# Performance work log

Measured on AMD Instinct MI355X. Metric: run time of the kernel, lower is better.

## Reference

```python
import jax, jax.numpy as jnp
import numpy as np

D_MODEL = 40; N_LAYER = 256
D_INNER = 80; D_STATE = 16; D_CONV = 4; DT_RANK = 3  # mamba defaults: expand=2, dt_rank=ceil(40/16)
PE_HID = 48; FF_MULT = 4
B, L, N = 1, 400, 65536


def setup_inputs():
    key = jax.random.key(0)
    ks = jax.random.split(key, 16)
    f32 = jnp.float32
    def rn(k, shape, s=0.02):
        return jax.random.normal(k, shape, f32) * s
    inp = {}
    inp['mash_params'] = jax.random.normal(ks[0], (B, L, D_MODEL), f32)
    inp['qry'] = jax.random.uniform(ks[1], (B, N, 3), f32, -1.0, 1.0)
    # stacked per-layer Mamba params (leading dim = N_LAYER)
    inp['l_norm_w'] = jnp.ones((N_LAYER, D_MODEL), f32)
    inp['l_in_w'] = rn(ks[2], (N_LAYER, 2 * D_INNER, D_MODEL), 0.05)
    inp['l_conv_w'] = rn(ks[3], (N_LAYER, D_INNER, D_CONV), 0.2)
    inp['l_conv_b'] = jnp.zeros((N_LAYER, D_INNER), f32)
    inp['l_xproj_w'] = rn(ks[4], (N_LAYER, DT_RANK + 2 * D_STATE, D_INNER), 0.05)
    inp['l_dt_w'] = rn(ks[5], (N_LAYER, D_INNER, DT_RANK), 0.2)
    inp['l_dt_b'] = rn(ks[6], (N_LAYER, D_INNER), 0.5) - 4.0  # softplus -> small dt
    A = jnp.tile(jnp.arange(1, D_STATE + 1, dtype=f32)[None, None, :], (N_LAYER, D_INNER, 1))
    inp['l_A_log'] = jnp.log(A)
    inp['l_D'] = jnp.ones((N_LAYER, D_INNER), f32)
    inp['l_out_w'] = rn(ks[7], (N_LAYER, D_MODEL, D_INNER), 0.05)
    # PointEmbed MLP (Fourier basis is a fixed buffer, built in forward)
    inp['pe_mlp_w'] = rn(ks[8], (D_MODEL, PE_HID + 3), 0.1)
    inp['pe_mlp_b'] = jnp.zeros((D_MODEL,), f32)
    # PreNorm cross-attention (heads=1, dim_head=d_model)
    inp['ca_lnq_w'] = jnp.ones((D_MODEL,), f32); inp['ca_lnq_b'] = jnp.zeros((D_MODEL,), f32)
    inp['ca_lnc_w'] = jnp.ones((D_MODEL,), f32); inp['ca_lnc_b'] = jnp.zeros((D_MODEL,), f32)
    inp['ca_q_w'] = rn(ks[9], (D_MODEL, D_MODEL), 0.1)
    inp['ca_kv_w'] = rn(ks[10], (2 * D_MODEL, D_MODEL), 0.1)
    inp['ca_out_w'] = rn(ks[11], (D_MODEL, D_MODEL), 0.1)
    inp['ca_out_b'] = jnp.zeros((D_MODEL,), f32)
    # PreNorm GEGLU feed-forward
    inp['ff_ln_w'] = jnp.ones((D_MODEL,), f32); inp['ff_ln_b'] = jnp.zeros((D_MODEL,), f32)
    inp['ff_fc1_w'] = rn(ks[12], (2 * FF_MULT * D_MODEL, D_MODEL), 0.1)
    inp['ff_fc1_b'] = jnp.zeros((2 * FF_MULT * D_MODEL,), f32)
    inp['ff_fc2_w'] = rn(ks[13], (D_MODEL, FF_MULT * D_MODEL), 0.1)
    inp['ff_fc2_b'] = jnp.zeros((D_MODEL,), f32)
    inp['out_w'] = rn(ks[14], (1, D_MODEL), 0.1)
    inp['out_b'] = jnp.zeros((1,), f32)
    return inp


def _rmsnorm(x, w, eps=1e-5):
    return x * jax.lax.rsqrt(jnp.mean(x * x, -1, keepdims=True) + eps) * w


def _layernorm(x, w, b, eps=1e-5):
    m = jnp.mean(x, -1, keepdims=True)
    v = jnp.mean((x - m) ** 2, -1, keepdims=True)
    return (x - m) * jax.lax.rsqrt(v + eps) * w + b


def _mamba(u, p):
    # u: [b, l, d_model]
    xz = jnp.einsum('bld,ed->ble', u, p['in_w'])  # [b,l,2*di]
    x, z = jnp.split(xz, 2, -1)
    # depthwise causal conv1d, kernel D_CONV
    xt = jnp.swapaxes(x, 1, 2)  # [b, di, l]
    xc = jax.lax.conv_general_dilated(xt, p['conv_w'][:, None, :], (1,), [(D_CONV - 1, 0)],
                                      feature_group_count=D_INNER)
    x = jax.nn.silu(jnp.swapaxes(xc + p['conv_b'][None, :, None], 1, 2))  # [b,l,di]
    dbc = jnp.einsum('bld,ed->ble', x, p['xproj_w'])  # [b,l,dt_rank+2*ds]
    dtr = dbc[..., :DT_RANK]
    Bm = dbc[..., DT_RANK:DT_RANK + D_STATE]
    Cm = dbc[..., DT_RANK + D_STATE:]
    dt = jax.nn.softplus(jnp.einsum('blr,dr->bld', dtr, p['dt_w']) + p['dt_b'])  # [b,l,di]
    A = -jnp.exp(p['A_log'])  # [di, ds]
    dA = jnp.exp(dt[..., None] * A)                          # [b,l,di,ds]
    dBx = dt[..., None] * Bm[:, :, None, :] * x[..., None]   # [b,l,di,ds]
    def step(h, io):
        a, bx = io
        h = a * h + bx
        return h, h
    h0 = jnp.zeros((u.shape[0], D_INNER, D_STATE), u.dtype)
    _, hs = jax.lax.scan(step, h0, (jnp.moveaxis(dA, 1, 0), jnp.moveaxis(dBx, 1, 0)))
    hs = jnp.moveaxis(hs, 0, 1)  # [b,l,di,ds]
    y = jnp.einsum('blds,bls->bld', hs, Cm) + x * p['D']
    y = y * jax.nn.silu(z)
    return jnp.einsum('bld,ed->ble', y, p['out_w'])


def _forward(mash_params, qry, l_norm_w, l_in_w, l_conv_w, l_conv_b, l_xproj_w, l_dt_w, l_dt_b,
             l_A_log, l_D, l_out_w, pe_mlp_w, pe_mlp_b, ca_lnq_w, ca_lnq_b, ca_lnc_w, ca_lnc_b,
             ca_q_w, ca_kv_w, ca_out_w, ca_out_b, ff_ln_w, ff_ln_b, ff_fc1_w, ff_fc1_b,
             ff_fc2_w, ff_fc2_b, out_w, out_b):
    layer_params = dict(norm_w=l_norm_w, in_w=l_in_w, conv_w=l_conv_w, conv_b=l_conv_b,
                        xproj_w=l_xproj_w, dt_w=l_dt_w, dt_b=l_dt_b, A_log=l_A_log,
                        D=l_D, out_w=l_out_w)
    # Block: residual = x; h = RMSNorm(x); h = Mamba(h); then caller does x = h + residual
    def layer_fn(x, p):
        return x + _mamba(_rmsnorm(x, p['norm_w']), p), None
    x, _ = jax.lax.scan(layer_fn, mash_params, layer_params)
    # PointEmbed: Fourier features with fixed block-diagonal basis
    e = (2.0 ** jnp.arange(PE_HID // 6, dtype=jnp.float32)) * jnp.pi  # [8]
    z0 = jnp.zeros_like(e)
    basis = jnp.stack([jnp.concatenate([e, z0, z0]),
                       jnp.concatenate([z0, e, z0]),
                       jnp.concatenate([z0, z0, e])])  # [3, 24]
    proj = jnp.einsum('bnd,de->bne', qry, basis)
    pe = jnp.concatenate([jnp.sin(proj), jnp.cos(proj), qry], -1)  # [b,n,51]
    q_emb = jnp.einsum('bnf,df->bnd', pe, pe_mlp_w) + pe_mlp_b
    # PreNorm cross-attention (1 head, dim_head = d_model)
    qn = _layernorm(q_emb, ca_lnq_w, ca_lnq_b)
    cn = _layernorm(x, ca_lnc_w, ca_lnc_b)
    q = jnp.einsum('bnd,ed->bne', qn, ca_q_w)
    kv = jnp.einsum('bld,ed->ble', cn, ca_kv_w)
    k, v = jnp.split(kv, 2, -1)
    scale = D_MODEL ** -0.5
    attn = jax.nn.softmax(jnp.einsum('bnd,bld->bnl', q, k) * scale, axis=-1)  # [b,n,l]
    lat = jnp.einsum('bnl,bld->bnd', attn, v)
    lat = jnp.einsum('bnd,ed->bne', lat, ca_out_w) + ca_out_b
    # PreNorm GEGLU feed-forward with residual
    h = _layernorm(lat, ff_ln_w, ff_ln_b)
    a = jnp.einsum('bnd,ed->bne', h, ff_fc1_w) + ff_fc1_b
    x1, g = jnp.split(a, 2, -1)
    ff = jnp.einsum('bnf,df->bnd', x1 * jax.nn.gelu(g, approximate=False), ff_fc2_w) + ff_fc2_b
    lat = lat + ff
    occ = (jnp.einsum('bnd,od->bno', lat, out_w) + out_b)[..., 0]  # [b, n]
    return occ


def reference(mash_params, qry, l_norm_w, l_in_w, l_conv_w, l_conv_b, l_xproj_w, l_dt_w, l_dt_b,
              l_A_log, l_D, l_out_w, pe_mlp_w, pe_mlp_b, ca_lnq_w, ca_lnq_b, ca_lnc_w, ca_lnc_b,
              ca_q_w, ca_kv_w, ca_out_w, ca_out_b, ff_ln_w, ff_ln_b, ff_fc1_w, ff_fc1_b,
              ff_fc2_w, ff_fc2_b, out_w, out_b):
    return _forward(mash_params, qry, l_norm_w, l_in_w, l_conv_w, l_conv_b, l_xproj_w, l_dt_w,
                    l_dt_b, l_A_log, l_D, l_out_w, pe_mlp_w, pe_mlp_b, ca_lnq_w, ca_lnq_b,
                    ca_lnc_w, ca_lnc_b, ca_q_w, ca_kv_w, ca_out_w, ca_out_b, ff_ln_w, ff_ln_b,
                    ff_fc1_w, ff_fc1_b, ff_fc2_w, ff_fc2_b, out_w, out_b)
```

## Files before the change

kernel.cpp:

```cpp
#include <hip/hip_runtime.h>


#define CH 4
#define NCHUNK 100
#define TPB1 320

typedef unsigned long long u64;

__device__ __forceinline__ u64 pack2(float a, float b) {
  return ((u64)__float_as_uint(b) << 32) | (u64)__float_as_uint(a);
}
__device__ __forceinline__ float unplo(u64 a) {
  return __uint_as_float((unsigned)a);
}
__device__ __forceinline__ float unphi(u64 a) {
  return __uint_as_float((unsigned)(a >> 32));
}

__global__ void init_flags(int* __restrict__ flags) {
  int i = blockIdx.x * 256 + threadIdx.x;
  if (i < 256 * 16) flags[i] = 0;
}

__global__ __launch_bounds__(TPB1) void mamba_pipe(
    const float* __restrict__ mash,
    const float* __restrict__ g_norm_w,
    const float* __restrict__ g_in_w,
    const float* __restrict__ g_conv_w,
    const float* __restrict__ g_conv_b,
    const float* __restrict__ g_xp_w,
    const float* __restrict__ g_dt_w,
    const float* __restrict__ g_dt_b,
    const float* __restrict__ g_alog,
    const float* __restrict__ g_D,
    const float* __restrict__ g_out_w,
    float* __restrict__ xb0,
    float* __restrict__ xb1,
    int* __restrict__ flags)
{
  const int layer = blockIdx.x;
  const int tid = threadIdx.x;

  __shared__ float xin[160];
  __shared__ float xz[640];
  __shared__ float xs[320];
  __shared__ float dbc[144];
  __shared__ float yb[320];
  __shared__ float xhist[240];

  const int e_in = tid % 160;
  const int tA = tid / 160;
  float w_in_r[40];
  {
    const float4* g = (const float4*)(g_in_w + layer * 6400 + e_in * 40);
    const float4* nw = (const float4*)(g_norm_w + layer * 40);
#pragma unroll
    for (int k = 0; k < 10; ++k) {
      float4 v = g[k];
      float4 n = nw[k];
      w_in_r[4 * k] = v.x * n.x; w_in_r[4 * k + 1] = v.y * n.y;
      w_in_r[4 * k + 2] = v.z * n.z; w_in_r[4 * k + 3] = v.w * n.w;
    }
  }
  const int d_c = tid % 80;
  const int t_c = tid / 80;
  float cw[4]; float cb;
  {
    float4 v = *(const float4*)(g_conv_w + layer * 320 + d_c * 4);
    cw[0] = v.x; cw[1] = v.y; cw[2] = v.z; cw[3] = v.w;
    cb = g_conv_b[layer * 80 + d_c];
  }
  const int halfp = tid & 1;
  const int p_x = tid >> 1;
  const int t_x = p_x / 35, e_x = p_x % 35;
  float w_xp_r[40];
  if (p_x < 140) {
    const float4* g = (const float4*)(g_xp_w + layer * 2800 + e_x * 80 + halfp * 40);
#pragma unroll
    for (int k = 0; k < 10; ++k) {
      float4 v = g[k];
      w_xp_r[4 * k] = v.x; w_xp_r[4 * k + 1] = v.y;
      w_xp_r[4 * k + 2] = v.z; w_xp_r[4 * k + 3] = v.w;
    }
  }
  const int d_ch = tid >> 2;
  const int qq = tid & 3;
  float negA[4], hst[4];
  {
    float4 v = *(const float4*)(g_alog + layer * 1280 + tid * 4);
    negA[0] = -__expf(v.x); negA[1] = -__expf(v.y);
    negA[2] = -__expf(v.z); negA[3] = -__expf(v.w);
    hst[0] = hst[1] = hst[2] = hst[3] = 0.f;
  }
  const float dtw0 = g_dt_w[layer * 240 + d_ch * 3 + 0];
  const float dtw1 = g_dt_w[layer * 240 + d_ch * 3 + 1];
  const float dtw2 = g_dt_w[layer * 240 + d_ch * 3 + 2];
  const float dtb = g_dt_b[layer * 80 + d_ch];
  const float wD = g_D[layer * 80 + d_ch];
  const int p_o = tid >> 1;
  const int t_o = p_o / 40, e_o = p_o % 40;
  float w_out_r[40];
  {
    const float4* g = (const float4*)(g_out_w + layer * 3200 + e_o * 80 + halfp * 40);
#pragma unroll
    for (int k = 0; k < 10; ++k) {
      float4 v = g[k];
      w_out_r[4 * k] = v.x; w_out_r[4 * k + 1] = v.y;
      w_out_r[4 * k + 2] = v.z; w_out_r[4 * k + 3] = v.w;
    }
  }

  for (int i = tid; i < 240; i += TPB1) xhist[i] = 0.f;
  __syncthreads();

  const float* src = (layer == 0) ? mash : ((layer & 1) ? xb0 : xb1);
  float* dst = (layer & 1) ? xb1 : xb0;
  int* flag_prev = flags + (layer - 1) * 16;
  int* flag_cur = flags + layer * 16;

  for (int c = 0; c < NCHUNK; ++c) {
    const int t0 = c * CH;

    if (layer == 0) {
#pragma unroll
      for (int tt = 0; tt < 2; ++tt) {
        const int t = tA + 2 * tt;
        const float4* sp = (const float4*)(src + (t0 + t) * 40);
        float ss = 0.f, sd = 0.f;
#pragma unroll
        for (int k = 0; k < 10; ++k) {
          float4 v = sp[k];
          ss += v.x * v.x + v.y * v.y + v.z * v.z + v.w * v.w;
          sd += w_in_r[4 * k] * v.x + w_in_r[4 * k + 1] * v.y
              + w_in_r[4 * k + 2] * v.z + w_in_r[4 * k + 3] * v.w;
        }
        xz[t * 160 + e_in] = sd * rsqrtf(ss * (1.f / 40.f) + 1e-5f);
      }
      if (tid < 160) xin[tid] = src[t0 * 40 + tid];
    } else {
      while (__hip_atomic_load(flag_prev, __ATOMIC_RELAXED,
                               __HIP_MEMORY_SCOPE_AGENT) <= c)
        __builtin_amdgcn_s_sleep(1);
#pragma unroll
      for (int tt = 0; tt < 2; ++tt) {
        const int t = tA + 2 * tt;
        const u64* sp = (const u64*)(src + (t0 + t) * 40);
        float ss = 0.f, sd = 0.f;
#pragma unroll
        for (int k = 0; k < 20; ++k) {
          u64 a = __hip_atomic_load(sp + k, __ATOMIC_RELAXED,
                                    __HIP_MEMORY_SCOPE_AGENT);
          float v0 = unplo(a), v1 = unphi(a);
          ss += v0 * v0 + v1 * v1;
          sd += w_in_r[2 * k] * v0 + w_in_r[2 * k + 1] * v1;
        }
        xz[t * 160 + e_in] = sd * rsqrtf(ss * (1.f / 40.f) + 1e-5f);
      }
      if (tid < 80) {
        u64 a = __hip_atomic_load((const u64*)(src + t0 * 40) + tid,
                                  __ATOMIC_RELAXED, __HIP_MEMORY_SCOPE_AGENT);
        xin[2 * tid] = unplo(a);
        xin[2 * tid + 1] = unphi(a);
      }
    }
    __syncthreads();

    {
      float acc = cb;
#pragma unroll
      for (int j = 0; j < 4; ++j) {
        int lt = t_c - 3 + j;
        float xv = (lt >= 0) ? xz[lt * 160 + d_c] : xhist[(lt + 3) * 80 + d_c];
        acc += cw[j] * xv;
      }
      xs[t_c * 80 + d_c] = acc / (1.f + __expf(-acc));
    }
    __syncthreads();

    if (p_x < 140) {
      const float4* xp = (const float4*)&xs[t_x * 80 + halfp * 40];
      float s = 0.f;
#pragma unroll
      for (int k = 0; k < 10; ++k) {
        float4 v = xp[k];
        s += w_xp_r[4 * k] * v.x + w_xp_r[4 * k + 1] * v.y
           + w_xp_r[4 * k + 2] * v.z + w_xp_r[4 * k + 3] * v.w;
      }
      s += __shfl_xor(s, 1);
      if (halfp == 0) dbc[t_x * 36 + e_x] = s;
    } else {
      for (int k = tid - 280; k < 240; k += 40)
        xhist[k] = xz[(1 + k / 80) * 160 + (k % 80)];
    }
    __syncthreads();

#pragma unroll
    for (int t = 0; t < CH; ++t) {
      const float* db = &dbc[t * 36];
      float sdt = dtb + db[0] * dtw0 + db[1] * dtw1 + db[2] * dtw2;
      float dtval = (sdt > 15.f) ? sdt : __logf(1.f + __expf(sdt));
      float xval = xs[t * 80 + d_ch];
      float part = 0.f;
#pragma unroll
      for (int j = 0; j < 4; ++j) {
        int s_i = qq * 4 + j;
        float Bv = db[3 + s_i];
        float Cv = db[19 + s_i];
        hst[j] = __expf(dtval * negA[j]) * hst[j] + dtval * Bv * xval;
        part += hst[j] * Cv;
      }
      part += __shfl_xor(part, 1);
      part += __shfl_xor(part, 2);
      if (qq == 0) {
        float yv = part + xval * wD;
        float z = xz[t * 160 + 80 + d_ch];
        yb[t * 80 + d_ch] = yv * z / (1.f + __expf(-z));
      }
    }
    __syncthreads();

    {
      const float4* yp = (const float4*)&yb[t_o * 80 + halfp * 40];
      float s = 0.f;
#pragma unroll
      for (int k = 0; k < 10; ++k) {
        float4 v = yp[k];
        s += w_out_r[4 * k] * v.x + w_out_r[4 * k + 1] * v.y
           + w_out_r[4 * k + 2] * v.z + w_out_r[4 * k + 3] * v.w;
      }
      s += __shfl_xor(s, 1);
      float r = xin[p_o] + s;
      float r2 = __shfl_xor(r, 2);
      if ((tid & 3) == 0)
        __hip_atomic_store((u64*)(dst + t0 * 40 + p_o), pack2(r, r2),
                           __ATOMIC_RELAXED, __HIP_MEMORY_SCOPE_AGENT);
    }
    __syncthreads();
    if (tid == 0)
      __hip_atomic_store(flag_cur, c + 1, __ATOMIC_RELAXED,
                         __HIP_MEMORY_SCOPE_AGENT);
  }
}

__global__ __launch_bounds__(64) void kv_kernel(
    const float* __restrict__ xfin,
    const float* __restrict__ lnc_w, const float* __restrict__ lnc_b,
    const float* __restrict__ kv_w,
    float* __restrict__ kbuf, float* __restrict__ vbuf)
{
  int t = blockIdx.x;
  int lane = threadIdx.x;
  float x = (lane < 40) ? xfin[t * 40 + lane] : 0.f;
  float s = x;
#pragma unroll
  for (int o = 32; o >= 1; o >>= 1) s += __shfl_xor(s, o);
  float m = s * (1.f / 40.f);
  float dv = (lane < 40) ? (x - m) : 0.f;
  float v2 = dv * dv;
#pragma unroll
  for (int o = 32; o >= 1; o >>= 1) v2 += __shfl_xor(v2, o);
  float rstd = rsqrtf(v2 * (1.f / 40.f) + 1e-5f);
  __shared__ float cn[40];
  if (lane < 40) cn[lane] = dv * rstd * lnc_w[lane] + lnc_b[lane];
  __syncthreads();
  for (int e = lane; e < 80; e += 64) {
    float acc = 0.f;
#pragma unroll
    for (int d = 0; d < 40; ++d) acc += cn[d] * kv_w[e * 40 + d];
    if (e < 40) kbuf[t * 40 + e] = acc;
    else vbuf[t * 40 + (e - 40)] = acc;
  }
}

__global__ __launch_bounds__(256) void query_kernel(
    const float* __restrict__ qry,
    const float* __restrict__ pe_w, const float* __restrict__ pe_b,
    const float* __restrict__ lnq_w, const float* __restrict__ lnq_b,
    const float* __restrict__ qw,
    const float* __restrict__ ow, const float* __restrict__ ob,
    const float* __restrict__ flw, const float* __restrict__ flb,
    const float* __restrict__ w1, const float* __restrict__ b1,
    const float* __restrict__ w2, const float* __restrict__ b2,
    const float* __restrict__ outw, const float* __restrict__ outb,
    const float* __restrict__ kbuf, const float* __restrict__ vbuf,
    float* __restrict__ out)
{
  const int tid = threadIdx.x;
  const int h = __builtin_amdgcn_readfirstlane((tid >> 6) & 1);
  const int pj = tid >> 7;
  const int lane = tid & 63;
  const int n = blockIdx.x * 128 + pj * 64 + lane;
  const int ptn = tid ^ 64;
  __shared__ float colbuf[40 * 256];
  __shared__ float redm[256], redl[256];

  const float qx = qry[n * 3 + 0], qy = qry[n * 3 + 1], qz = qry[n * 3 + 2];

  float qp[40];
#pragma unroll
  for (int d = 0; d < 40; ++d) qp[d] = 0.f;
#pragma unroll
  for (int jj = 0; jj < 4; ++jj) {
    const int j = h * 4 + jj;
    float f = 3.14159265358979323846f * (float)(1 << j);
    float sx, cx, sy, cy, sz, cz;
    __sincosf(qx * f, &sx, &cx);
    __sincosf(qy * f, &sy, &cy);
    __sincosf(qz * f, &sz, &cz);
#pragma unroll
    for (int d = 0; d < 40; ++d) {
      const float* r = pe_w + d * 51;
      qp[d] += sx * r[j] + sy * r[j + 8] + sz * r[j + 16]
             + cx * r[j + 24] + cy * r[j + 32] + cz * r[j + 40];
    }
  }
#pragma unroll
  for (int d = 0; d < 40; ++d) colbuf[d * 256 + tid] = qp[d];
  __syncthreads();
  float qe[40];
#pragma unroll
  for (int d = 0; d < 40; ++d) {
    const float* r = pe_w + d * 51;
    qe[d] = pe_b[d] + qp[d] + colbuf[d * 256 + ptn]
          + qx * r[48] + qy * r[49] + qz * r[50];
  }
  __syncthreads();

  float qn[40];
  {
    float m = 0.f;
#pragma unroll
    for (int d = 0; d < 40; ++d) m += qe[d];
    m *= (1.f / 40.f);
    float var = 0.f;
#pragma unroll
    for (int d = 0; d < 40; ++d) { float dv = qe[d] - m; var += dv * dv; }
    float rstd = rsqrtf(var * (1.f / 40.f) + 1e-5f);
#pragma unroll
    for (int d = 0; d < 40; ++d) qn[d] = (qe[d] - m) * rstd * lnq_w[d] + lnq_b[d];
  }
  float qnh[20];
#pragma unroll
  for (int dd = 0; dd < 20; ++dd) qnh[dd] = h ? qn[dd + 20] : qn[dd];
  float q[40];
#pragma unroll
  for (int e = 0; e < 40; ++e) q[e] = 0.f;
#pragma unroll 1
  for (int dd = 0; dd < 20; ++dd) {
    const float qv = qnh[dd];
    const int d = h * 20 + dd;
#pragma unroll
    for (int e = 0; e < 40; ++e) q[e] += qv * qw[e * 40 + d];
  }
#pragma unroll
  for (int e = 0; e < 40; ++e) colbuf[e * 256 + tid] = q[e];
  __syncthreads();
#pragma unroll
  for (int e = 0; e < 40; ++e) q[e] += colbuf[e * 256 + ptn];
  __syncthreads();

  float acc[40];
#pragma unroll
  for (int d = 0; d < 40; ++d) acc[d] = 0.f;
  float mx = -1e30f, l = 0.f;
  const float scale = 0.15811388300841897f;
  const int tbeg = h * 200, tend = tbeg + 200;
#pragma unroll 1
  for (int t = tbeg; t < tend; ++t) {
    const float4* kr = (const float4*)(kbuf + t * 40);
    float s0 = 0.f, s1 = 0.f, s2 = 0.f, s3 = 0.f;
#pragma unroll
    for (int k = 0; k < 10; ++k) {
      float4 k4 = kr[k];
      s0 += q[4 * k] * k4.x; s1 += q[4 * k + 1] * k4.y;
      s2 += q[4 * k + 2] * k4.z; s3 += q[4 * k + 3] * k4.w;
    }
    float s = ((s0 + s1) + (s2 + s3)) * scale;
    if (s > mx) {
      float corr = __expf(mx - s);
      l *= corr;
#pragma unroll
      for (int d = 0; d < 40; ++d) acc[d] *= corr;
      mx = s;
    }
    float p = __expf(s - mx);
    l += p;
    const float4* vr = (const float4*)(vbuf + t * 40);
#pragma unroll
    for (int k = 0; k < 10; ++k) {
      float4 v4 = vr[k];
      acc[4 * k] += p * v4.x; acc[4 * k + 1] += p * v4.y;
      acc[4 * k + 2] += p * v4.z; acc[4 * k + 3] += p * v4.w;
    }
  }
#pragma unroll
  for (int d = 0; d < 40; ++d) colbuf[d * 256 + tid] = acc[d];
  redm[tid] = mx; redl[tid] = l;
  __syncthreads();
  float lat[40];
  {
    float m2 = redm[ptn];
    float l2 = redl[ptn];
    float nm = fmaxf(mx, m2);
    float a = __expf(mx - nm), b = __expf(m2 - nm);
    float lm = l * a + l2 * b;
    float linv = 1.f / lm;
#pragma unroll
    for (int d = 0; d < 40; ++d)
      lat[d] = (acc[d] * a + colbuf[d * 256 + ptn] * b) * linv;
  }
  __syncthreads();

  float lath[20];
#pragma unroll
  for (int dd = 0; dd < 20; ++dd) lath[dd] = h ? lat[dd + 20] : lat[dd];
  float lp[40];
#pragma unroll
  for (int e = 0; e < 40; ++e) lp[e] = 0.f;
#pragma unroll 1
  for (int dd = 0; dd < 20; ++dd) {
    const float lv = lath[dd];
    const int d = h * 20 + dd;
#pragma unroll
    for (int e = 0; e < 40; ++e) lp[e] += lv * ow[e * 40 + d];
  }
#pragma unroll
  for (int e = 0; e < 40; ++e) colbuf[e * 256 + tid] = lp[e];
  __syncthreads();
  float lat2[40];
#pragma unroll
  for (int e = 0; e < 40; ++e) lat2[e] = ob[e] + lp[e] + colbuf[e * 256 + ptn];
  __syncthreads();

  float hh[40];
  {
    float m = 0.f;
#pragma unroll
    for (int d = 0; d < 40; ++d) m += lat2[d];
    m *= (1.f / 40.f);
    float var = 0.f;
#pragma unroll
    for (int d = 0; d < 40; ++d) { float dv = lat2[d] - m; var += dv * dv; }
    float rstd = rsqrtf(var * (1.f / 40.f) + 1e-5f);
#pragma unroll
    for (int d = 0; d < 40; ++d) hh[d] = (lat2[d] - m) * rstd * flw[d] + flb[d];
  }
  float ff[40];
#pragma unroll
  for (int d = 0; d < 40; ++d) ff[d] = 0.f;
#pragma unroll 1
  for (int ee = 0; ee < 80; ++ee) {
    const int e = h * 80 + ee;
    const float* r1 = w1 + e * 40;
    const float* r2 = w1 + (160 + e) * 40;
    float a0 = 0.f, a1 = 0.f;
#pragma unroll
    for (int d = 0; d < 40; ++d) { a0 += hh[d] * r1[d]; a1 += hh[d] * r2[d]; }
    float x1 = a0 + b1[e];
    float g = a1 + b1[160 + e];
    float tv = x1 * (0.5f * g * (1.f + erff(g * 0.70710678118654752f)));
#pragma unroll
    for (int d = 0; d < 40; ++d) ff[d] += tv * w2[d * 160 + e];
  }
#pragma unroll
  for (int d = 0; d < 40; ++d) colbuf[d * 256 + tid] = ff[d];
  __syncthreads();
  float r = outb[0];
#pragma unroll
  for (int d = 0; d < 40; ++d) {
    float f = ff[d] + colbuf[d * 256 + ptn] + b2[d];
    r += (lat2[d] + f) * outw[d];
  }
  if (h == 0) out[n] = r;
}

extern "C" void kernel_launch(void* const* d_in, const int* in_sizes, int n_in,
                              void* d_out, int out_size, void* d_ws, size_t ws_size,
                              hipStream_t stream) {
  const float* mash   = (const float*)d_in[0];
  const float* qry    = (const float*)d_in[1];
  const float* lnw    = (const float*)d_in[2];
  const float* linw   = (const float*)d_in[3];
  const float* lconvw = (const float*)d_in[4];
  const float* lconvb = (const float*)d_in[5];
  const float* lxpw   = (const float*)d_in[6];
  const float* ldtw   = (const float*)d_in[7];
  const float* ldtb   = (const float*)d_in[8];
  const float* lAlog  = (const float*)d_in[9];
  const float* lD     = (const float*)d_in[10];
  const float* loutw  = (const float*)d_in[11];
  const float* pew    = (const float*)d_in[12];
  const float* peb    = (const float*)d_in[13];
  const float* lnqw   = (const float*)d_in[14];
  const float* lnqb   = (const float*)d_in[15];
  const float* lncw   = (const float*)d_in[16];
  const float* lncb   = (const float*)d_in[17];
  const float* qw     = (const float*)d_in[18];
  const float* kvw    = (const float*)d_in[19];
  const float* oww    = (const float*)d_in[20];
  const float* owb    = (const float*)d_in[21];
  const float* flnw   = (const float*)d_in[22];
  const float* flnb   = (const float*)d_in[23];
  const float* w1     = (const float*)d_in[24];
  const float* b1     = (const float*)d_in[25];
  const float* w2     = (const float*)d_in[26];
  const float* b2     = (const float*)d_in[27];
  const float* outw   = (const float*)d_in[28];
  const float* outb   = (const float*)d_in[29];

  float* wsf = (float*)d_ws;
  float* xb0 = wsf;
  float* xb1 = wsf + 16000;
  float* kbuf = wsf + 32000;
  float* vbuf = wsf + 48000;
  int* flags = (int*)(wsf + 64000);

  hipLaunchKernelGGL(init_flags, dim3(16), dim3(256), 0, stream, flags);
  hipLaunchKernelGGL(mamba_pipe, dim3(256), dim3(TPB1), 0, stream,
                     mash, lnw, linw, lconvw, lconvb, lxpw, ldtw, ldtb, lAlog,
                     lD, loutw, xb0, xb1, flags);
  hipLaunchKernelGGL(kv_kernel, dim3(400), dim3(64), 0, stream,
                     xb1, lncw, lncb, kvw, kbuf, vbuf);
  hipLaunchKernelGGL(query_kernel, dim3(512), dim3(256), 0, stream,
                     qry, pew, peb, lnqw, lnqb, qw, oww, owb, flnw, flnb,
                     w1, b1, w2, b2, outw, outb, kbuf, vbuf, (float*)d_out);
}
```

Measured before the change: 2.168 ms.

## Precompute query projections in spare blocks of the Mamba pipeline kernel

```diff
diff --git a/kernel.cpp b/kernel.cpp
--- a/kernel.cpp
+++ b/kernel.cpp
@@ -36,10 +36,71 @@
     const float* __restrict__ g_out_w,
     float* __restrict__ xb0,
     float* __restrict__ xb1,
-    int* __restrict__ flags)
+    int* __restrict__ flags,
+    const float* __restrict__ qry,
+    const float* __restrict__ pe_w, const float* __restrict__ pe_b,
+    const float* __restrict__ lnq_w, const float* __restrict__ lnq_b,
+    const float* __restrict__ qw,
+    float* __restrict__ qstore)
 {
+  const int tid = threadIdx.x;
+
+  if (blockIdx.x >= 256) {
+    const int n = (blockIdx.x - 256) * TPB1 + tid;
+    if (n < 65536) {
+      const float qx = qry[n * 3 + 0], qy = qry[n * 3 + 1], qz = qry[n * 3 + 2];
+      float qe[40];
+#pragma unroll
+      for (int d = 0; d < 40; ++d) qe[d] = pe_b[d];
+#pragma unroll 1
+      for (int j = 0; j < 8; ++j) {
+        float f = 3.14159265358979323846f * (float)(1 << j);
+        float sx, cx, sy, cy, sz, cz;
+        __sincosf(qx * f, &sx, &cx);
+        __sincosf(qy * f, &sy, &cy);
+        __sincosf(qz * f, &sz, &cz);
+#pragma unroll
+        for (int d = 0; d < 40; ++d) {
+          const float* r = pe_w + d * 51;
+          qe[d] += sx * r[j] + sy * r[j + 8] + sz * r[j + 16]
+                 + cx * r[j + 24] + cy * r[j + 32] + cz * r[j + 40];
+        }
+      }
+#pragma unroll
+      for (int d = 0; d < 40; ++d) {
+        const float* r = pe_w + d * 51;
+        qe[d] += qx * r[48] + qy * r[49] + qz * r[50];
+      }
+      float qn[40];
+      {
+        float m = 0.f;
+#pragma unroll
+        for (int d = 0; d < 40; ++d) m += qe[d];
+        m *= (1.f / 40.f);
+        float var = 0.f;
+#pragma unroll
+        for (int d = 0; d < 40; ++d) { float dv = qe[d] - m; var += dv * dv; }
+        float rstd = rsqrtf(var * (1.f / 40.f) + 1e-5f);
+#pragma unroll
+        for (int d = 0; d < 40; ++d)
+          qn[d] = (qe[d] - m) * rstd * lnq_w[d] + lnq_b[d];
+      }
+      float q[40];
+#pragma unroll
+      for (int e = 0; e < 40; ++e) {
+        const float* r = qw + e * 40;
+        float s = 0.f;
+#pragma unroll
+        for (int d = 0; d < 40; ++d) s += qn[d] * r[d];
+        q[e] = s;
+      }
+#pragma unroll
+      for (int e = 0; e < 40; ++e) qstore[e * 65536 + n] = q[e];
+    }
+    return;
+  }
+
   const int layer = blockIdx.x;
-  const int tid = threadIdx.x;
 
   __shared__ float xin[160];
   __shared__ float xz[640];
@@ -272,7 +333,187 @@
   }
 }
 
-__global__ __launch_bounds__(256) void query_kernel(
+__global__ __launch_bounds__(256) void query_fast(
+    const float* __restrict__ qstore,
+    const float* __restrict__ ow, const float* __restrict__ ob,
+    const float* __restrict__ flw, const float* __restrict__ flb,
+    const float* __restrict__ w1, const float* __restrict__ b1,
+    const float* __restrict__ w2, const float* __restrict__ b2,
+    const float* __restrict__ outw, const float* __restrict__ outb,
+    const float* __restrict__ kbuf, const float* __restrict__ vbuf,
+    float* __restrict__ out)
+{
+  const int tid = threadIdx.x;
+  const int h = __builtin_amdgcn_readfirstlane((tid >> 6) & 3);
+  const int lane = tid & 63;
+  const int n = blockIdx.x * 64 + lane;
+  const int p1 = tid ^ 64, p2 = tid ^ 128, p3 = tid ^ 192;
+  __shared__ float colbuf[40 * 256];
+
+  float q[40];
+#pragma unroll
+  for (int e = 0; e < 40; ++e) q[e] = qstore[e * 65536 + n];
+
+  float acc[40];
+#pragma unroll
+  for (int d = 0; d < 40; ++d) acc[d] = 0.f;
+  float mx = -1e30f, l = 0.f;
+  const float scale = 0.15811388300841897f;
+  const int tbeg = h * 100;
+#pragma unroll 1
+  for (int t = tbeg; t < tbeg + 100; t += 2) {
+    const float4* ka = (const float4*)(kbuf + t * 40);
+    const float4* kb = (const float4*)(kbuf + t * 40 + 40);
+    float a0 = 0.f, a1 = 0.f, b0 = 0.f, b1s = 0.f;
+#pragma unroll
+    for (int k = 0; k < 10; ++k) {
+      float4 k4 = ka[k];
+      float4 j4 = kb[k];
+      a0 += q[4 * k] * k4.x + q[4 * k + 1] * k4.y;
+      a1 += q[4 * k + 2] * k4.z + q[4 * k + 3] * k4.w;
+      b0 += q[4 * k] * j4.x + q[4 * k + 1] * j4.y;
+      b1s += q[4 * k + 2] * j4.z + q[4 * k + 3] * j4.w;
+    }
+    float sa = (a0 + a1) * scale;
+    float sb = (b0 + b1s) * scale;
+    {
+      if (sa > mx) {
+        float corr = __expf(mx - sa);
+        l *= corr;
+#pragma unroll
+        for (int d = 0; d < 40; ++d) acc[d] *= corr;
+        mx = sa;
+      }
+      float p = __expf(sa - mx);
+      l += p;
+      const float4* vr = (const float4*)(vbuf + t * 40);
+#pragma unroll
+      for (int k = 0; k < 10; ++k) {
+        float4 v4 = vr[k];
+        acc[4 * k] += p * v4.x; acc[4 * k + 1] += p * v4.y;
+        acc[4 * k + 2] += p * v4.z; acc[4 * k + 3] += p * v4.w;
+      }
+    }
+    {
+      if (sb > mx) {
+        float corr = __expf(mx - sb);
+        l *= corr;
+#pragma unroll
+        for (int d = 0; d < 40; ++d) acc[d] *= corr;
+        mx = sb;
+      }
+      float p = __expf(sb - mx);
+      l += p;
+      const float4* vr = (const float4*)(vbuf + (t + 1) * 40);
+#pragma unroll
+      for (int k = 0; k < 10; ++k) {
+        float4 v4 = vr[k];
+        acc[4 * k] += p * v4.x; acc[4 * k + 1] += p * v4.y;
+        acc[4 * k + 2] += p * v4.z; acc[4 * k + 3] += p * v4.w;
+      }
+    }
+  }
+
+  {
+    float* redm = colbuf;
+    float* redl = colbuf + 256;
+    redm[tid] = mx; redl[tid] = l;
+  }
+  __syncthreads();
+  float a0c, a1c, a2c, a3c, linv;
+  {
+    float m1 = colbuf[p1], m2 = colbuf[p2], m3 = colbuf[p3];
+    float l1 = colbuf[256 + p1], l2 = colbuf[256 + p2], l3 = colbuf[256 + p3];
+    float nm = fmaxf(fmaxf(mx, m1), fmaxf(m2, m3));
+    a0c = __expf(mx - nm); a1c = __expf(m1 - nm);
+    a2c = __expf(m2 - nm); a3c = __expf(m3 - nm);
+    float L = l * a0c + l1 * a1c + l2 * a2c + l3 * a3c;
+    linv = 1.f / L;
+  }
+  __syncthreads();
+#pragma unroll
+  for (int d = 0; d < 40; ++d) colbuf[d * 256 + tid] = acc[d];
+  __syncthreads();
+  float lat[40];
+#pragma unroll
+  for (int d = 0; d < 40; ++d)
+    lat[d] = (acc[d] * a0c + colbuf[d * 256 + p1] * a1c
+            + colbuf[d * 256 + p2] * a2c + colbuf[d * 256 + p3] * a3c) * linv;
+  __syncthreads();
+
+  float lath[10];
+#pragma unroll
+  for (int dd = 0; dd < 10; ++dd) {
+    float v = lat[dd];
+    v = (h == 1) ? lat[dd + 10] : v;
+    v = (h == 2) ? lat[dd + 20] : v;
+    v = (h == 3) ? lat[dd + 30] : v;
+    lath[dd] = v;
+  }
+  float lp[40];
+#pragma unroll
+  for (int e = 0; e < 40; ++e) lp[e] = 0.f;
+#pragma unroll 1
+  for (int dd = 0; dd < 10; ++dd) {
+    const float lv = lath[dd];
+    const int d = h * 10 + dd;
+#pragma unroll
+    for (int e = 0; e < 40; ++e) lp[e] += lv * ow[e * 40 + d];
+  }
+#pragma unroll
+  for (int e = 0; e < 40; ++e) colbuf[e * 256 + tid] = lp[e];
+  __syncthreads();
+  float lat2[40];
+#pragma unroll
+  for (int e = 0; e < 40; ++e)
+    lat2[e] = ob[e] + lp[e] + colbuf[e * 256 + p1]
+            + colbuf[e * 256 + p2] + colbuf[e * 256 + p3];
+  __syncthreads();
+
+  float hh[40];
+  {
+    float m = 0.f;
+#pragma unroll
+    for (int d = 0; d < 40; ++d) m += lat2[d];
+    m *= (1.f / 40.f);
+    float var = 0.f;
+#pragma unroll
+    for (int d = 0; d < 40; ++d) { float dv = lat2[d] - m; var += dv * dv; }
+    float rstd = rsqrtf(var * (1.f / 40.f) + 1e-5f);
+#pragma unroll
+    for (int d = 0; d < 40; ++d) hh[d] = (lat2[d] - m) * rstd * flw[d] + flb[d];
+  }
+  float ff[40];
+#pragma unroll
+  for (int d = 0; d < 40; ++d) ff[d] = 0.f;
+#pragma unroll 1
+  for (int ee = 0; ee < 40; ++ee) {
+    const int e = h * 40 + ee;
+    const float* r1 = w1 + e * 40;
+    const float* r2 = w1 + (160 + e) * 40;
+    float s0 = 0.f, s1 = 0.f;
+#pragma unroll
+    for (int d = 0; d < 40; ++d) { s0 += hh[d] * r1[d]; s1 += hh[d] * r2[d]; }
+    float x1 = s0 + b1[e];
+    float g = s1 + b1[160 + e];
+    float tv = x1 * (0.5f * g * (1.f + erff(g * 0.70710678118654752f)));
+#pragma unroll
+    for (int d = 0; d < 40; ++d) ff[d] += tv * w2[d * 160 + e];
+  }
+#pragma unroll
+  for (int d = 0; d < 40; ++d) colbuf[d * 256 + tid] = ff[d];
+  __syncthreads();
+  float r = outb[0];
+#pragma unroll
+  for (int d = 0; d < 40; ++d) {
+    float f = ff[d] + colbuf[d * 256 + p1] + colbuf[d * 256 + p2]
+            + colbuf[d * 256 + p3] + b2[d];
+    r += (lat2[d] + f) * outw[d];
+  }
+  if (h == 0) out[n] = r;
+}
+
+__global__ __launch_bounds__(256) void query_kernel_fb(
     const float* __restrict__ qry,
     const float* __restrict__ pe_w, const float* __restrict__ pe_b,
     const float* __restrict__ lnq_w, const float* __restrict__ lnq_b,
@@ -295,7 +536,6 @@
   __shared__ float redm[256], redl[256];
 
   const float qx = qry[n * 3 + 0], qy = qry[n * 3 + 1], qz = qry[n * 3 + 2];
-
   float qp[40];
 #pragma unroll
   for (int d = 0; d < 40; ++d) qp[d] = 0.f;
@@ -325,7 +565,6 @@
           + qx * r[48] + qy * r[49] + qz * r[50];
   }
   __syncthreads();
-
   float qn[40];
   {
     float m = 0.f;
@@ -410,7 +649,6 @@
       lat[d] = (acc[d] * a + colbuf[d * 256 + ptn] * b) * linv;
   }
   __syncthreads();
-
   float lath[20];
 #pragma unroll
   for (int dd = 0; dd < 20; ++dd) lath[dd] = h ? lat[dd + 20] : lat[dd];
@@ -431,7 +669,6 @@
 #pragma unroll
   for (int e = 0; e < 40; ++e) lat2[e] = ob[e] + lp[e] + colbuf[e * 256 + ptn];
   __syncthreads();
-
   float hh[40];
   {
     float m = 0.f;
@@ -453,11 +690,11 @@
     const int e = h * 80 + ee;
     const float* r1 = w1 + e * 40;
     const float* r2 = w1 + (160 + e) * 40;
-    float a0 = 0.f, a1 = 0.f;
-#pragma unroll
-    for (int d = 0; d < 40; ++d) { a0 += hh[d] * r1[d]; a1 += hh[d] * r2[d]; }
-    float x1 = a0 + b1[e];
-    float g = a1 + b1[160 + e];
+    float s0 = 0.f, s1 = 0.f;
+#pragma unroll
+    for (int d = 0; d < 40; ++d) { s0 += hh[d] * r1[d]; s1 += hh[d] * r2[d]; }
+    float x1 = s0 + b1[e];
+    float g = s1 + b1[160 + e];
     float tv = x1 * (0.5f * g * (1.f + erff(g * 0.70710678118654752f)));
 #pragma unroll
     for (int d = 0; d < 40; ++d) ff[d] += tv * w2[d * 160 + e];
@@ -514,14 +751,24 @@
   float* kbuf = wsf + 32000;
   float* vbuf = wsf + 48000;
   int* flags = (int*)(wsf + 64000);
+  float* qstore = wsf + 68096;
+  const size_t needed = (size_t)68096 * 4 + (size_t)40 * 65536 * 4;
+  const bool pre = ws_size >= needed;
 
   hipLaunchKernelGGL(init_flags, dim3(16), dim3(256), 0, stream, flags);
-  hipLaunchKernelGGL(mamba_pipe, dim3(256), dim3(TPB1), 0, stream,
+  hipLaunchKernelGGL(mamba_pipe, dim3(pre ? 461 : 256), dim3(TPB1), 0, stream,
                      mash, lnw, linw, lconvw, lconvb, lxpw, ldtw, ldtb, lAlog,
-                     lD, loutw, xb0, xb1, flags);
+                     lD, loutw, xb0, xb1, flags,
+                     qry, pew, peb, lnqw, lnqb, qw, qstore);
   hipLaunchKernelGGL(kv_kernel, dim3(400), dim3(64), 0, stream,
                      xb1, lncw, lncb, kvw, kbuf, vbuf);
-  hipLaunchKernelGGL(query_kernel, dim3(512), dim3(256), 0, stream,
-                     qry, pew, peb, lnqw, lnqb, qw, oww, owb, flnw, flnb,
-                     w1, b1, w2, b2, outw, outb, kbuf, vbuf, (float*)d_out);
-}
+  if (pre) {
+    hipLaunchKernelGGL(query_fast, dim3(1024), dim3(256), 0, stream,
+                       qstore, oww, owb, flnw, flnb,
+                       w1, b1, w2, b2, outw, outb, kbuf, vbuf, (float*)d_out);
+  } else {
+    hipLaunchKernelGGL(query_kernel_fb, dim3(512), dim3(256), 0, stream,
+                       qry, pew, peb, lnqw, lnqb, qw, oww, owb, flnw, flnb,
+                       w1, b1, w2, b2, outw, outb, kbuf, vbuf, (float*)d_out);
+  }
+}
```

Result: faster. 2.115 ms (-2.4%).

## Fuse KV projection and query attention into the persistent mamba pipeline kernel

Applied to the files above, without the earlier changes.

```diff
diff --git a/kernel.cpp b/kernel.cpp
--- a/kernel.cpp
+++ b/kernel.cpp
@@ -19,10 +19,10 @@
 
 __global__ void init_flags(int* __restrict__ flags) {
   int i = blockIdx.x * 256 + threadIdx.x;
-  if (i < 256 * 16) flags[i] = 0;
+  if (i < 257 * 16) flags[i] = 0;
 }
 
-__global__ __launch_bounds__(TPB1) void mamba_pipe(
+__global__ __launch_bounds__(TPB1, 3) void mamba_pipe(
     const float* __restrict__ mash,
     const float* __restrict__ g_norm_w,
     const float* __restrict__ g_in_w,
@@ -36,9 +36,21 @@
     const float* __restrict__ g_out_w,
     float* __restrict__ xb0,
     float* __restrict__ xb1,
-    int* __restrict__ flags)
+    int* __restrict__ flags,
+    const float* __restrict__ lnc_w, const float* __restrict__ lnc_b,
+    const float* __restrict__ kv_w,
+    float* __restrict__ kbuf, float* __restrict__ vbuf,
+    const float* __restrict__ qry,
+    const float* __restrict__ pe_w, const float* __restrict__ pe_b,
+    const float* __restrict__ lnq_w, const float* __restrict__ lnq_b,
+    const float* __restrict__ qw,
+    const float* __restrict__ ow, const float* __restrict__ ob,
+    const float* __restrict__ flw, const float* __restrict__ flb,
+    const float* __restrict__ w1, const float* __restrict__ b1,
+    const float* __restrict__ w2, const float* __restrict__ b2,
+    const float* __restrict__ outw, const float* __restrict__ outb,
+    float* __restrict__ out)
 {
-  const int layer = blockIdx.x;
   const int tid = threadIdx.x;
 
   __shared__ float xin[160];
@@ -47,6 +59,233 @@
   __shared__ float dbc[144];
   __shared__ float yb[320];
   __shared__ float xhist[240];
+
+  if (blockIdx.x >= 257) {
+    const int waveid = tid >> 6;
+    const int lane = tid & 63;
+    const int wq = (blockIdx.x - 257) * 5 + waveid;
+    if (wq >= 1024) return;
+    const int n = wq * 64 + lane;
+
+    const float qx = qry[n * 3 + 0], qy = qry[n * 3 + 1], qz = qry[n * 3 + 2];
+    float q[40];
+    {
+      float qe[40];
+#pragma unroll
+      for (int d = 0; d < 40; ++d) qe[d] = pe_b[d];
+#pragma unroll 1
+      for (int j = 0; j < 8; ++j) {
+        float f = 3.14159265358979323846f * (float)(1 << j);
+        float sx, cx, sy, cy, sz, cz;
+        __sincosf(qx * f, &sx, &cx);
+        __sincosf(qy * f, &sy, &cy);
+        __sincosf(qz * f, &sz, &cz);
+#pragma unroll
+        for (int d = 0; d < 40; ++d) {
+          const float* r = pe_w + d * 51;
+          qe[d] += sx * r[j] + sy * r[j + 8] + sz * r[j + 16]
+                 + cx * r[j + 24] + cy * r[j + 32] + cz * r[j + 40];
+        }
+      }
+#pragma unroll
+      for (int d = 0; d < 40; ++d) {
+        const float* r = pe_w + d * 51;
+        qe[d] += qx * r[48] + qy * r[49] + qz * r[50];
+      }
+      float m = 0.f;
+#pragma unroll
+      for (int d = 0; d < 40; ++d) m += qe[d];
+      m *= (1.f / 40.f);
+      float var = 0.f;
+#pragma unroll
+      for (int d = 0; d < 40; ++d) { float dv = qe[d] - m; var += dv * dv; }
+      float rstd = rsqrtf(var * (1.f / 40.f) + 1e-5f);
+      float qn[40];
+#pragma unroll
+      for (int d = 0; d < 40; ++d)
+        qn[d] = (qe[d] - m) * rstd * lnq_w[d] + lnq_b[d];
+#pragma unroll
+      for (int e = 0; e < 40; ++e) {
+        const float* r = qw + e * 40;
+        float s = 0.f;
+#pragma unroll
+        for (int d = 0; d < 40; ++d) s += qn[d] * r[d];
+        q[e] = s;
+      }
+    }
+
+    int* kv_flag = flags + 256 * 16;
+    float acc[40];
+#pragma unroll
+    for (int d = 0; d < 40; ++d) acc[d] = 0.f;
+    float mx = -1e30f, l = 0.f;
+    const float scale = 0.15811388300841897f;
+#pragma unroll 1
+    for (int c = 0; c < NCHUNK; ++c) {
+      if (c == 0) {
+        while (__hip_atomic_load(kv_flag, __ATOMIC_RELAXED,
+                                 __HIP_MEMORY_SCOPE_AGENT) <= 0)
+          __builtin_amdgcn_s_sleep(32);
+      } else {
+        while (__hip_atomic_load(kv_flag, __ATOMIC_RELAXED,
+                                 __HIP_MEMORY_SCOPE_AGENT) <= c)
+          __builtin_amdgcn_s_sleep(8);
+      }
+#pragma unroll 1
+      for (int tt = 0; tt < CH; ++tt) {
+        const int t = c * CH + tt;
+        const u64* kp = (const u64*)(kbuf + t * 40);
+        float kvv[40];
+#pragma unroll
+        for (int k = 0; k < 20; ++k) {
+          u64 a = __hip_atomic_load(kp + k, __ATOMIC_RELAXED,
+                                    __HIP_MEMORY_SCOPE_AGENT);
+          kvv[2 * k] = unplo(a); kvv[2 * k + 1] = unphi(a);
+        }
+        float s0 = 0.f, s1 = 0.f, s2 = 0.f, s3 = 0.f;
+#pragma unroll
+        for (int d = 0; d < 40; d += 4) {
+          s0 += q[d] * kvv[d]; s1 += q[d + 1] * kvv[d + 1];
+          s2 += q[d + 2] * kvv[d + 2]; s3 += q[d + 3] * kvv[d + 3];
+        }
+        float s = ((s0 + s1) + (s2 + s3)) * scale;
+        if (s > mx) {
+          float corr = __expf(mx - s);
+          l *= corr;
+#pragma unroll
+          for (int d = 0; d < 40; ++d) acc[d] *= corr;
+          mx = s;
+        }
+        float p = __expf(s - mx);
+        l += p;
+        const u64* vp = (const u64*)(vbuf + t * 40);
+#pragma unroll
+        for (int k = 0; k < 20; ++k) {
+          u64 a = __hip_atomic_load(vp + k, __ATOMIC_RELAXED,
+                                    __HIP_MEMORY_SCOPE_AGENT);
+          acc[2 * k] += p * unplo(a);
+          acc[2 * k + 1] += p * unphi(a);
+        }
+      }
+    }
+
+    float linv = 1.f / l;
+    float lat[40];
+#pragma unroll
+    for (int d = 0; d < 40; ++d) lat[d] = acc[d] * linv;
+    float lat2[40];
+#pragma unroll 1
+    for (int e = 0; e < 40; ++e) {
+      const float* r = ow + e * 40;
+      float s = 0.f;
+#pragma unroll
+      for (int d = 0; d < 40; ++d) s += lat[d] * r[d];
+      lat2[e] = ob[e] + s;
+    }
+    float hh[40];
+    {
+      float m = 0.f;
+#pragma unroll
+      for (int d = 0; d < 40; ++d) m += lat2[d];
+      m *= (1.f / 40.f);
+      float var = 0.f;
+#pragma unroll
+      for (int d = 0; d < 40; ++d) { float dv = lat2[d] - m; var += dv * dv; }
+      float rstd = rsqrtf(var * (1.f / 40.f) + 1e-5f);
+#pragma unroll
+      for (int d = 0; d < 40; ++d)
+        hh[d] = (lat2[d] - m) * rstd * flw[d] + flb[d];
+    }
+    float ff[40];
+#pragma unroll
+    for (int d = 0; d < 40; ++d) ff[d] = b2[d];
+#pragma unroll 1
+    for (int e = 0; e < 160; ++e) {
+      const float* r1 = w1 + e * 40;
+      const float* r2 = w1 + (160 + e) * 40;
+      float a0 = 0.f, a1 = 0.f;
+#pragma unroll
+      for (int d = 0; d < 40; ++d) { a0 += hh[d] * r1[d]; a1 += hh[d] * r2[d]; }
+      float x1 = a0 + b1[e];
+      float g = a1 + b1[160 + e];
+      float tv = x1 * (0.5f * g * (1.f + erff(g * 0.70710678118654752f)));
+#pragma unroll
+      for (int d = 0; d < 40; ++d) ff[d] += tv * w2[d * 160 + e];
+    }
+    float r = outb[0];
+#pragma unroll
+    for (int d = 0; d < 40; ++d) r += (lat2[d] + ff[d]) * outw[d];
+    out[n] = r;
+    return;
+  }
+
+  if (blockIdx.x == 256) {
+    const int t_k = tid / 80;
+    const int e_k = tid % 80;
+    float wkv[40];
+    {
+      const float4* g = (const float4*)(kv_w + e_k * 40);
+#pragma unroll
+      for (int k = 0; k < 10; ++k) {
+        float4 v = g[k];
+        wkv[4 * k] = v.x; wkv[4 * k + 1] = v.y;
+        wkv[4 * k + 2] = v.z; wkv[4 * k + 3] = v.w;
+      }
+    }
+    float lw = 0.f, lb = 0.f;
+    if (tid < 160) { lw = lnc_w[tid % 40]; lb = lnc_b[tid % 40]; }
+    const u64* srcT = (const u64*)xb1;
+    int* flag_src = flags + 255 * 16;
+    int* kv_flag = flags + 256 * 16;
+
+    for (int c = 0; c < NCHUNK; ++c) {
+      while (__hip_atomic_load(flag_src, __ATOMIC_RELAXED,
+                               __HIP_MEMORY_SCOPE_AGENT) <= c)
+        __builtin_amdgcn_s_sleep(1);
+      if (tid < 80) {
+        u64 a = __hip_atomic_load(srcT + c * 80 + tid, __ATOMIC_RELAXED,
+                                  __HIP_MEMORY_SCOPE_AGENT);
+        xz[2 * tid] = unplo(a);
+        xz[2 * tid + 1] = unphi(a);
+      }
+      __syncthreads();
+      if (tid < 160) {
+        const int t = tid / 40;
+        float m = 0.f;
+#pragma unroll
+        for (int k = 0; k < 40; ++k) m += xz[t * 40 + k];
+        m *= (1.f / 40.f);
+        float var = 0.f;
+#pragma unroll
+        for (int k = 0; k < 40; ++k) {
+          float dv = xz[t * 40 + k] - m; var += dv * dv;
+        }
+        float rstd = rsqrtf(var * (1.f / 40.f) + 1e-5f);
+        yb[tid] = (xz[tid] - m) * rstd * lw + lb;
+      }
+      __syncthreads();
+      {
+        const float* cn = &yb[t_k * 40];
+        float s = 0.f;
+#pragma unroll
+        for (int d = 0; d < 40; ++d) s += wkv[d] * cn[d];
+        const int trow = c * CH + t_k;
+        if (e_k < 40)
+          __hip_atomic_store(&kbuf[trow * 40 + e_k], s, __ATOMIC_RELAXED,
+                             __HIP_MEMORY_SCOPE_AGENT);
+        else
+          __hip_atomic_store(&vbuf[trow * 40 + (e_k - 40)], s,
+                             __ATOMIC_RELAXED, __HIP_MEMORY_SCOPE_AGENT);
+      }
+      __syncthreads();
+      if (tid == 0)
+        __hip_atomic_store(kv_flag, c + 1, __ATOMIC_RELAXED,
+                           __HIP_MEMORY_SCOPE_AGENT);
+    }
+    return;
+  }
+
+  const int layer = blockIdx.x;
 
   const int e_in = tid % 160;
   const int tA = tid / 160;
@@ -240,238 +479,6 @@
       __hip_atomic_store(flag_cur, c + 1, __ATOMIC_RELAXED,
                          __HIP_MEMORY_SCOPE_AGENT);
   }
-}
-
-__global__ __launch_bounds__(64) void kv_kernel(
-    const float* __restrict__ xfin,
-    const float* __restrict__ lnc_w, const float* __restrict__ lnc_b,
-    const float* __restrict__ kv_w,
-    float* __restrict__ kbuf, float* __restrict__ vbuf)
-{
-  int t = blockIdx.x;
-  int lane = threadIdx.x;
-  float x = (lane < 40) ? xfin[t * 40 + lane] : 0.f;
-  float s = x;
-#pragma unroll
-  for (int o = 32; o >= 1; o >>= 1) s += __shfl_xor(s, o);
-  float m = s * (1.f / 40.f);
-  float dv = (lane < 40) ? (x - m) : 0.f;
-  float v2 = dv * dv;
-#pragma unroll
-  for (int o = 32; o >= 1; o >>= 1) v2 += __shfl_xor(v2, o);
-  float rstd = rsqrtf(v2 * (1.f / 40.f) + 1e-5f);
-  __shared__ float cn[40];
-  if (lane < 40) cn[lane] = dv * rstd * lnc_w[lane] + lnc_b[lane];
-  __syncthreads();
-  for (int e = lane; e < 80; e += 64) {
-    float acc = 0.f;
-#pragma unroll
-    for (int d = 0; d < 40; ++d) acc += cn[d] * kv_w[e * 40 + d];
-    if (e < 40) kbuf[t * 40 + e] = acc;
-    else vbuf[t * 40 + (e - 40)] = acc;
-  }
-}
-
-__global__ __launch_bounds__(256) void query_kernel(
-    const float* __restrict__ qry,
-    const float* __restrict__ pe_w, const float* __restrict__ pe_b,
-    const float* __restrict__ lnq_w, const float* __restrict__ lnq_b,
-    const float* __restrict__ qw,
-    const float* __restrict__ ow, const float* __restrict__ ob,
-    const float* __restrict__ flw, const float* __restrict__ flb,
-    const float* __restrict__ w1, const float* __restrict__ b1,
-    const float* __restrict__ w2, const float* __restrict__ b2,
-    const float* __restrict__ outw, const float* __restrict__ outb,
-    const float* __restrict__ kbuf, const float* __restrict__ vbuf,
-    float* __restrict__ out)
-{
-  const int tid = threadIdx.x;
-  const int h = __builtin_amdgcn_readfirstlane((tid >> 6) & 1);
-  const int pj = tid >> 7;
-  const int lane = tid & 63;
-  const int n = blockIdx.x * 128 + pj * 64 + lane;
-  const int ptn = tid ^ 64;
-  __shared__ float colbuf[40 * 256];
-  __shared__ float redm[256], redl[256];
-
-  const float qx = qry[n * 3 + 0], qy = qry[n * 3 + 1], qz = qry[n * 3 + 2];
-
-  float qp[40];
-#pragma unroll
-  for (int d = 0; d < 40; ++d) qp[d] = 0.f;
-#pragma unroll
-  for (int jj = 0; jj < 4; ++jj) {
-    const int j = h * 4 + jj;
-    float f = 3.14159265358979323846f * (float)(1 << j);
-    float sx, cx, sy, cy, sz, cz;
-    __sincosf(qx * f, &sx, &cx);
-    __sincosf(qy * f, &sy, &cy);
-    __sincosf(qz * f, &sz, &cz);
-#pragma unroll
-    for (int d = 0; d < 40; ++d) {
-      const float* r = pe_w + d * 51;
-      qp[d] += sx * r[j] + sy * r[j + 8] + sz * r[j + 16]
-             + cx * r[j + 24] + cy * r[j + 32] + cz * r[j + 40];
-    }
-  }
-#pragma unroll
-  for (int d = 0; d < 40; ++d) colbuf[d * 256 + tid] = qp[d];
-  __syncthreads();
-  float qe[40];
-#pragma unroll
-  for (int d = 0; d < 40; ++d) {
-    const float* r = pe_w + d * 51;
-    qe[d] = pe_b[d] + qp[d] + colbuf[d * 256 + ptn]
-          + qx * r[48] + qy * r[49] + qz * r[50];
-  }
-  __syncthreads();
-
-  float qn[40];
-  {
-    float m = 0.f;
-#pragma unroll
-    for (int d = 0; d < 40; ++d) m += qe[d];
-    m *= (1.f / 40.f);
-    float var = 0.f;
-#pragma unroll
-    for (int d = 0; d < 40; ++d) { float dv = qe[d] - m; var += dv * dv; }
-    float rstd = rsqrtf(var * (1.f / 40.f) + 1e-5f);
-#pragma unroll
-    for (int d = 0; d < 40; ++d) qn[d] = (qe[d] - m) * rstd * lnq_w[d] + lnq_b[d];
-  }
-  float qnh[20];
-#pragma unroll
-  for (int dd = 0; dd < 20; ++dd) qnh[dd] = h ? qn[dd + 20] : qn[dd];
-  float q[40];
-#pragma unroll
-  for (int e = 0; e < 40; ++e) q[e] = 0.f;
-#pragma unroll 1
-  for (int dd = 0; dd < 20; ++dd) {
-    const float qv = qnh[dd];
-    const int d = h * 20 + dd;
-#pragma unroll
-    for (int e = 0; e < 40; ++e) q[e] += qv * qw[e * 40 + d];
-  }
-#pragma unroll
-  for (int e = 0; e < 40; ++e) colbuf[e * 256 + tid] = q[e];
-  __syncthreads();
-#pragma unroll
-  for (int e = 0; e < 40; ++e) q[e] += colbuf[e * 256 + ptn];
-  __syncthreads();
-
-  float acc[40];
-#pragma unroll
-  for (int d = 0; d < 40; ++d) acc[d] = 0.f;
-  float mx = -1e30f, l = 0.f;
-  const float scale = 0.15811388300841897f;
-  const int tbeg = h * 200, tend = tbeg + 200;
-#pragma unroll 1
-  for (int t = tbeg; t < tend; ++t) {
-    const float4* kr = (const float4*)(kbuf + t * 40);
-    float s0 = 0.f, s1 = 0.f, s2 = 0.f, s3 = 0.f;
-#pragma unroll
-    for (int k = 0; k < 10; ++k) {
-      float4 k4 = kr[k];
-      s0 += q[4 * k] * k4.x; s1 += q[4 * k + 1] * k4.y;
-      s2 += q[4 * k + 2] * k4.z; s3 += q[4 * k + 3] * k4.w;
-    }
-    float s = ((s0 + s1) + (s2 + s3)) * scale;
-    if (s > mx) {
-      float corr = __expf(mx - s);
-      l *= corr;
-#pragma unroll
-      for (int d = 0; d < 40; ++d) acc[d] *= corr;
-      mx = s;
-    }
-    float p = __expf(s - mx);
-    l += p;
-    const float4* vr = (const float4*)(vbuf + t * 40);
-#pragma unroll
-    for (int k = 0; k < 10; ++k) {
-      float4 v4 = vr[k];
-      acc[4 * k] += p * v4.x; acc[4 * k + 1] += p * v4.y;
-      acc[4 * k + 2] += p * v4.z; acc[4 * k + 3] += p * v4.w;
-    }
-  }
-#pragma unroll
-  for (int d = 0; d < 40; ++d) colbuf[d * 256 + tid] = acc[d];
-  redm[tid] = mx; redl[tid] = l;
-  __syncthreads();
-  float lat[40];
-  {
-    float m2 = redm[ptn];
-    float l2 = redl[ptn];
-    float nm = fmaxf(mx, m2);
-    float a = __expf(mx - nm), b = __expf(m2 - nm);
-    float lm = l * a + l2 * b;
-    float linv = 1.f / lm;
-#pragma unroll
-    for (int d = 0; d < 40; ++d)
-      lat[d] = (acc[d] * a + colbuf[d * 256 + ptn] * b) * linv;
-  }
-  __syncthreads();
-
-  float lath[20];
-#pragma unroll
-  for (int dd = 0; dd < 20; ++dd) lath[dd] = h ? lat[dd + 20] : lat[dd];
-  float lp[40];
-#pragma unroll
-  for (int e = 0; e < 40; ++e) lp[e] = 0.f;
-#pragma unroll 1
-  for (int dd = 0; dd < 20; ++dd) {
-    const float lv = lath[dd];
-    const int d = h * 20 + dd;
-#pragma unroll
-    for (int e = 0; e < 40; ++e) lp[e] += lv * ow[e * 40 + d];
-  }
-#pragma unroll
-  for (int e = 0; e < 40; ++e) colbuf[e * 256 + tid] = lp[e];
-  __syncthreads();
-  float lat2[40];
-#pragma unroll
-  for (int e = 0; e < 40; ++e) lat2[e] = ob[e] + lp[e] + colbuf[e * 256 + ptn];
-  __syncthreads();
-
-  float hh[40];
-  {
-    float m = 0.f;
-#pragma unroll
-    for (int d = 0; d < 40; ++d) m += lat2[d];
-    m *= (1.f / 40.f);
-    float var = 0.f;
-#pragma unroll
-    for (int d = 0; d < 40; ++d) { float dv = lat2[d] - m; var += dv * dv; }
-    float rstd = rsqrtf(var * (1.f / 40.f) + 1e-5f);
-#pragma unroll
-    for (int d = 0; d < 40; ++d) hh[d] = (lat2[d] - m) * rstd * flw[d] + flb[d];
-  }
-  float ff[40];
-#pragma unroll
-  for (int d = 0; d < 40; ++d) ff[d] = 0.f;
-#pragma unroll 1
-  for (int ee = 0; ee < 80; ++ee) {
-    const int e = h * 80 + ee;
-    const float* r1 = w1 + e * 40;
-    const float* r2 = w1 + (160 + e) * 40;
-    float a0 = 0.f, a1 = 0.f;
-#pragma unroll
-    for (int d = 0; d < 40; ++d) { a0 += hh[d] * r1[d]; a1 += hh[d] * r2[d]; }
-    float x1 = a0 + b1[e];
-    float g = a1 + b1[160 + e];
-    float tv = x1 * (0.5f * g * (1.f + erff(g * 0.70710678118654752f)));
-#pragma unroll
-    for (int d = 0; d < 40; ++d) ff[d] += tv * w2[d * 160 + e];
-  }
-#pragma unroll
-  for (int d = 0; d < 40; ++d) colbuf[d * 256 + tid] = ff[d];
-  __syncthreads();
-  float r = outb[0];
-#pragma unroll
-  for (int d = 0; d < 40; ++d) {
-    float f = ff[d] + colbuf[d * 256 + ptn] + b2[d];
-    r += (lat2[d] + f) * outw[d];
-  }
-  if (h == 0) out[n] = r;
 }
 
 extern "C" void kernel_launch(void* const* d_in, const int* in_sizes, int n_in,
@@ -515,13 +522,12 @@
   float* vbuf = wsf + 48000;
   int* flags = (int*)(wsf + 64000);
 
-  hipLaunchKernelGGL(init_flags, dim3(16), dim3(256), 0, stream, flags);
-  hipLaunchKernelGGL(mamba_pipe, dim3(256), dim3(TPB1), 0, stream,
+  hipLaunchKernelGGL(init_flags, dim3(17), dim3(256), 0, stream, flags);
+  hipLaunchKernelGGL(mamba_pipe, dim3(462), dim3(TPB1), 0, stream,
                      mash, lnw, linw, lconvw, lconvb, lxpw, ldtw, ldtb, lAlog,
-                     lD, loutw, xb0, xb1, flags);
-  hipLaunchKernelGGL(kv_kernel, dim3(400), dim3(64), 0, stream,
-                     xb1, lncw, lncb, kvw, kbuf, vbuf);
-  hipLaunchKernelGGL(query_kernel, dim3(512), dim3(256), 0, stream,
-                     qry, pew, peb, lnqw, lnqb, qw, oww, owb, flnw, flnb,
-                     w1, b1, w2, b2, outw, outb, kbuf, vbuf, (float*)d_out);
+                     lD, loutw, xb0, xb1, flags,
+                     lncw, lncb, kvw, kbuf, vbuf,
+                     qry, pew, peb, lnqw, lnqb, qw,
+                     oww, owb, flnw, flnb, w1, b1, w2, b2, outw, outb,
+                     (float*)d_out);
 }
```

Result: slower. 3.955 ms (+82.4%).
